# Optimization experiments

Hardware: AMD Instinct MI355X
Metric: run time of the kernel (lower is better)

Reference implementation:

```python
import jax, jax.numpy as jnp
import numpy as np

B, C, N_IN = 32, 64, 10475
N_OUT = 2619
NNZ = 8 * N_OUT  # ~8 barycentric entries per output vertex


def setup_inputs() -> dict:
    key = jax.random.key(0)
    k1, k2, k3, k4 = jax.random.split(key, 4)
    x = jax.random.normal(k1, (B, C, N_IN), dtype=jnp.float32)
    # Sparse mesh-sampling operator M [N_OUT, N_IN] in COO form,
    # sparsity pattern shared across the whole batch.
    M_rows = jax.random.randint(k2, (NNZ,), 0, N_OUT, dtype=jnp.int32)
    M_cols = jax.random.randint(k3, (NNZ,), 0, N_IN, dtype=jnp.int32)
    M_vals = jax.random.uniform(k4, (NNZ,), dtype=jnp.float32)
    return {"x": x, "M_rows": M_rows, "M_cols": M_cols, "M_vals": M_vals}


def reference(x, M_rows, M_cols, M_vals):
    """Batched spmm: out[b, c, r] = sum_{k: M_rows[k]==r} M_vals[k] * x[b, c, M_cols[k]].

    Equivalent to the torch module: for each batch element, M @ x[b].T, stacked,
    then transposed back to [B, C, N_OUT]. Here the batch loop is fused into a
    single gather + segment_sum that reuses the shared sparsity pattern.
    """
    # Gather source vertex features for every nnz entry: [B, C, NNZ]
    g = x[:, :, M_cols] * M_vals
    # segment_sum reduces over the leading axis -> move nnz to front
    g = jnp.moveaxis(g, 2, 0)                                   # [NNZ, B, C]
    out = jax.ops.segment_sum(g, M_rows, num_segments=N_OUT)    # [N_OUT, B, C]
    return jnp.moveaxis(out, 0, 2)                              # [B, C, N_OUT]
```

## Files before the change

### kernel.cpp

```cpp
#include <hip/hip_runtime.h>
#include <hip/hip_fp16.h>
#include <stdint.h>

#define Bdim   32
#define Cdim   64
#define N_IN   10475
#define N_OUT  2619
#define NNZ    (8 * N_OUT)
#define MAIN_BLK 512
#define CHUNK  41
#define ENT_PAD (CHUNK * MAIN_BLK)
#define SMALL_BLK 256
#define Gpair  2
#define NBLK   (Bdim * Cdim / Gpair)

#define SENT_META 0x0FFF0000u

#define OFF_OFFS   10480
#define OFF_ENT    20976
#define OFF_ELAST  (OFF_ENT + 20 * MAIN_BLK * 16)
#define WS_NEEDED  (OFF_ELAST + MAIN_BLK * 8)

__global__ __launch_bounds__(SMALL_BLK) void init_ws(
        int* __restrict__ cursor, uint2* __restrict__ ent2,
        uint2* __restrict__ entLast) {
    int i = blockIdx.x * SMALL_BLK + threadIdx.x;
    if (i < N_OUT) cursor[i] = 0;
    if (i < ENT_PAD - NNZ) {
        int p  = NNZ + i;
        int tt = p / CHUNK;
        int ss = p - tt * CHUNK;
        uint2 sv = make_uint2(SENT_META, 0u);
        if (ss < 40) ent2[(ss >> 1) * (MAIN_BLK * 2) + tt * 2 + (ss & 1)] = sv;
        else         entLast[tt] = sv;
    }
}

__global__ __launch_bounds__(SMALL_BLK) void hist_rows(
        const int* __restrict__ rows, int* __restrict__ counts) {
    int k = blockIdx.x * SMALL_BLK + threadIdx.x;
    if (k < NNZ) atomicAdd(&counts[rows[k]], 1);
}

__global__ __launch_bounds__(1024) void scan_counts(
        int* __restrict__ counts, int* __restrict__ offsets) {
    __shared__ int wsum[16];
    const int t = threadIdx.x, lane = t & 63, w = t >> 6;
    const int base = t * 3;
    int v0 = (base + 0 < N_OUT) ? counts[base + 0] : 0;
    int v1 = (base + 1 < N_OUT) ? counts[base + 1] : 0;
    int v2 = (base + 2 < N_OUT) ? counts[base + 2] : 0;
    int s = v0 + v1 + v2;
    const int tot = s;
    #pragma unroll
    for (int d = 1; d < 64; d <<= 1) {
        int n = __shfl_up(s, d);
        if (lane >= d) s += n;
    }
    if (lane == 63) wsum[w] = s;
    __syncthreads();
    if (t < 16) {
        int ws_ = wsum[t];
        #pragma unroll
        for (int d = 1; d < 16; d <<= 1) {
            int n = __shfl_up(ws_, d);
            if (t >= d) ws_ += n;
        }
        wsum[t] = ws_;
    }
    __syncthreads();
    int excl = ((w > 0) ? wsum[w - 1] : 0) + (s - tot);
    if (base + 0 <= N_OUT) { offsets[base + 0] = excl; if (base + 0 < N_OUT) counts[base + 0] = excl; }
    excl += v0;
    if (base + 1 <= N_OUT) { offsets[base + 1] = excl; if (base + 1 < N_OUT) counts[base + 1] = excl; }
    excl += v1;
    if (base + 2 <= N_OUT) { offsets[base + 2] = excl; if (base + 2 < N_OUT) counts[base + 2] = excl; }
}

__global__ __launch_bounds__(SMALL_BLK) void scatter_entries(
        const int* __restrict__ rows, const int* __restrict__ cols,
        const float* __restrict__ vals,
        int* __restrict__ cursor, const int* __restrict__ offsets,
        uint2* __restrict__ ent2, uint2* __restrict__ entLast) {
    int k = blockIdx.x * SMALL_BLK + threadIdx.x;
    if (k < NNZ) {
        int r = rows[k];
        int p = atomicAdd(&cursor[r], 1);
        uint32_t flag = (p == offsets[r + 1] - 1) ? 0x80000000u : 0u;
        uint32_t meta = flag | ((uint32_t)r << 16) | ((uint32_t)cols[k] << 2);
        __half2 hv = __half2half2(__float2half(vals[k]));
        uint2 e = make_uint2(meta, *(uint32_t*)&hv);
        int t = p / CHUNK;
        int s = p - t * CHUNK;
        if (s < 40) ent2[(s >> 1) * (MAIN_BLK * 2) + t * 2 + (s & 1)] = e;
        else        entLast[t] = e;
    }
}

__global__ __launch_bounds__(MAIN_BLK, 6) void spmm_g2p(
        const float* __restrict__ x,
        const uint4* __restrict__ ent4,
        const uint2* __restrict__ entLast,
        float* __restrict__ out) {
    __shared__ __half2 xs2[N_IN];
    __shared__ __half2 out2[N_OUT];
    __shared__ int     wCarryRow[8];
    __shared__ int     wCarryVal[8];

    const int blk  = blockIdx.x;
    const int t    = threadIdx.x, lane = t & 63, w = t >> 6;
    const float* __restrict__ xr0 = x + (size_t)(Gpair * blk) * N_IN;
    const float* __restrict__ xr1 = xr0 + N_IN;

    uint4 c0 = ent4[0 * MAIN_BLK + t];
    uint4 c1 = ent4[1 * MAIN_BLK + t];
    uint4 c2 = ent4[2 * MAIN_BLK + t];
    uint4 c3 = ent4[3 * MAIN_BLK + t];
    const uint2 el = entLast[t];

    __half* xsh = (__half*)xs2;
    constexpr int NP = (N_IN - 1) / 2;
    #pragma unroll 2
    for (int p = t; p < NP; p += MAIN_BLK) {
        int c = 2 * p;
        float2 a = *(const float2*)(xr0 + c);
        xsh[2 * c]     = __float2half(a.x);
        xsh[2 * c + 2] = __float2half(a.y);
    }
    #pragma unroll 2
    for (int p = t; p < NP; p += MAIN_BLK) {
        int c = 2 * p + 1;
        float2 b = *(const float2*)(xr1 + c);
        xsh[2 * c + 1] = __float2half(b.x);
        xsh[2 * c + 3] = __float2half(b.y);
    }
    if (t == 0) xsh[2 * (N_IN - 1)] = __float2half(xr0[N_IN - 1]);
    if (t == 1) xsh[1]              = __float2half(xr1[0]);
    {
        const __half2 z = __half2half2(__float2half(0.f));
        #pragma unroll
        for (int i = t; i < N_OUT; i += MAIN_BLK) out2[i] = z;
    }
    __syncthreads();

    const __half2 hzero = __half2half2(__float2half(0.f));
    __half2 acc = hzero, facc = hzero;
    int firstRow = -1;

#define FEED(meta, vb) do {                                              \
        uint32_t xp = *(const uint32_t*)((const char*)xs2 + ((meta) & 0xFFFFu)); \
        acc = __hfma2(*(const __half2*)&(vb), *(const __half2*)&xp, acc); \
        if ((int)(meta) < 0) {                                           \
            int row_ = (int)(((meta) >> 16) & 0xFFFu);                   \
            if (firstRow < 0) { firstRow = row_; facc = acc; }           \
            else out2[row_] = acc;                                       \
            acc = hzero;                                                 \
        }                                                                \
    } while (0)

    #pragma unroll
    for (int jb = 0; jb < 5; ++jb) {
        uint4 n0, n1, n2, n3;
        if (jb < 4) {
            n0 = ent4[((jb + 1) * 4 + 0) * MAIN_BLK + t];
            n1 = ent4[((jb + 1) * 4 + 1) * MAIN_BLK + t];
            n2 = ent4[((jb + 1) * 4 + 2) * MAIN_BLK + t];
            n3 = ent4[((jb + 1) * 4 + 3) * MAIN_BLK + t];
        }
        FEED(c0.x, c0.y); FEED(c0.z, c0.w);
        FEED(c1.x, c1.y); FEED(c1.z, c1.w);
        FEED(c2.x, c2.y); FEED(c2.z, c2.w);
        FEED(c3.x, c3.y); FEED(c3.z, c3.w);
        if (jb < 4) { c0 = n0; c1 = n1; c2 = n2; c3 = n3; }
    }
    FEED(el.x, el.y);
#undef FEED

    const int carryRow = (int)((el.x >> 16) & 0xFFFu);
    const int cai = *(const int*)&acc;

    int pRow = __shfl_up(carryRow, 1);
    int pAi  = __shfl_up(cai, 1);
    if (lane == 63) { wCarryRow[w] = carryRow; wCarryVal[w] = cai; }
    __syncthreads();
    if (lane == 0) {
        pRow = (w > 0) ? wCarryRow[w - 1] : -1;
        pAi  = (w > 0) ? wCarryVal[w - 1] : 0;
    }

    if (firstRow >= 0 && firstRow < N_OUT) {
        if (pRow == firstRow) facc = __hadd2(facc, *(const __half2*)&pAi);
        out2[firstRow] = facc;
    }
    __syncthreads();

    float* __restrict__ o0 = out + (size_t)(Gpair * blk) * N_OUT;
    float* __restrict__ o1 = o0 + N_OUT;
    #pragma unroll
    for (int i = t; i < N_OUT; i += MAIN_BLK) {
        float2 vv = __half22float2(out2[i]);
        o0[i] = vv.x;
        o1[i] = vv.y;
    }
}

__global__ __launch_bounds__(SMALL_BLK) void spmm_raw(
        const float* __restrict__ x,
        const int* __restrict__ rows,
        const int* __restrict__ cols,
        const float* __restrict__ vals,
        float* __restrict__ out) {
    __shared__ float x_lds[N_IN];
    __shared__ float out_lds[N_OUT];
    const int bc = blockIdx.x;
    const float* __restrict__ xrow = x + (size_t)bc * N_IN;
    for (int i = threadIdx.x; i < N_IN; i += SMALL_BLK) x_lds[i] = xrow[i];
    for (int i = threadIdx.x; i < N_OUT; i += SMALL_BLK) out_lds[i] = 0.0f;
    __syncthreads();
    for (int k = threadIdx.x; k < NNZ; k += SMALL_BLK) {
        atomicAdd(&out_lds[rows[k]], vals[k] * x_lds[cols[k]]);
    }
    __syncthreads();
    float* __restrict__ orow = out + (size_t)bc * N_OUT;
    for (int i = threadIdx.x; i < N_OUT; i += SMALL_BLK) orow[i] = out_lds[i];
}

extern "C" void kernel_launch(void* const* d_in, const int* in_sizes, int n_in,
                              void* d_out, int out_size, void* d_ws, size_t ws_size,
                              hipStream_t stream) {
    const float* x    = (const float*)d_in[0];
    const int*   rows = (const int*)d_in[1];
    const int*   cols = (const int*)d_in[2];
    const float* vals = (const float*)d_in[3];
    float*       out  = (float*)d_out;

    if (ws_size >= (size_t)WS_NEEDED) {
        char*  ws      = (char*)d_ws;
        int*   cursor  = (int*)ws;
        int*   offsets = (int*)(ws + OFF_OFFS);
        uint2* ent2    = (uint2*)(ws + OFF_ENT);
        const uint4* ent4 = (const uint4*)(ws + OFF_ENT);
        uint2* entLast = (uint2*)(ws + OFF_ELAST);

        const int gi = (N_OUT + SMALL_BLK - 1) / SMALL_BLK;
        const int gk = (NNZ + SMALL_BLK - 1) / SMALL_BLK;

        init_ws<<<gi, SMALL_BLK, 0, stream>>>(cursor, ent2, entLast);
        hist_rows<<<gk, SMALL_BLK, 0, stream>>>(rows, cursor);
        scan_counts<<<1, 1024, 0, stream>>>(cursor, offsets);
        scatter_entries<<<gk, SMALL_BLK, 0, stream>>>(rows, cols, vals, cursor,
                                                      offsets, ent2, entLast);
        spmm_g2p<<<NBLK, MAIN_BLK, 0, stream>>>(x, ent4, entLast, out);
    } else {
        spmm_raw<<<Bdim * Cdim, SMALL_BLK, 0, stream>>>(x, rows, cols, vals, out);
    }
}
```

Measured before the change: 157.8 us.

## Fuse COO preprocessing into one single-block kernel and batch LDS gathers

```diff
diff --git a/kernel.cpp b/kernel.cpp
--- a/kernel.cpp
+++ b/kernel.cpp
@@ -16,40 +16,29 @@
 
 #define SENT_META 0x0FFF0000u
 
-#define OFF_OFFS   10480
-#define OFF_ENT    20976
-#define OFF_ELAST  (OFF_ENT + 20 * MAIN_BLK * 16)
+#define OFF_ELAST  (20 * MAIN_BLK * 16)
 #define WS_NEEDED  (OFF_ELAST + MAIN_BLK * 8)
 
-__global__ __launch_bounds__(SMALL_BLK) void init_ws(
-        int* __restrict__ cursor, uint2* __restrict__ ent2,
-        uint2* __restrict__ entLast) {
-    int i = blockIdx.x * SMALL_BLK + threadIdx.x;
-    if (i < N_OUT) cursor[i] = 0;
-    if (i < ENT_PAD - NNZ) {
-        int p  = NNZ + i;
-        int tt = p / CHUNK;
-        int ss = p - tt * CHUNK;
-        uint2 sv = make_uint2(SENT_META, 0u);
-        if (ss < 40) ent2[(ss >> 1) * (MAIN_BLK * 2) + tt * 2 + (ss & 1)] = sv;
-        else         entLast[tt] = sv;
-    }
-}
-
-__global__ __launch_bounds__(SMALL_BLK) void hist_rows(
-        const int* __restrict__ rows, int* __restrict__ counts) {
-    int k = blockIdx.x * SMALL_BLK + threadIdx.x;
-    if (k < NNZ) atomicAdd(&counts[rows[k]], 1);
-}
-
-__global__ __launch_bounds__(1024) void scan_counts(
-        int* __restrict__ counts, int* __restrict__ offsets) {
+__global__ __launch_bounds__(1024) void prep_all(
+        const int* __restrict__ rows, const int* __restrict__ cols,
+        const float* __restrict__ vals,
+        uint2* __restrict__ ent2, uint2* __restrict__ entLast) {
+    __shared__ int cnt[N_OUT];
+    __shared__ int lastpos[N_OUT];
     __shared__ int wsum[16];
+
     const int t = threadIdx.x, lane = t & 63, w = t >> 6;
+
+    for (int i = t; i < N_OUT; i += 1024) cnt[i] = 0;
+    __syncthreads();
+
+    for (int k = t; k < NNZ; k += 1024) atomicAdd(&cnt[rows[k]], 1);
+    __syncthreads();
+
     const int base = t * 3;
-    int v0 = (base + 0 < N_OUT) ? counts[base + 0] : 0;
-    int v1 = (base + 1 < N_OUT) ? counts[base + 1] : 0;
-    int v2 = (base + 2 < N_OUT) ? counts[base + 2] : 0;
+    int v0 = (base + 0 < N_OUT) ? cnt[base + 0] : 0;
+    int v1 = (base + 1 < N_OUT) ? cnt[base + 1] : 0;
+    int v2 = (base + 2 < N_OUT) ? cnt[base + 2] : 0;
     int s = v0 + v1 + v2;
     const int tot = s;
     #pragma unroll
@@ -70,30 +59,32 @@
     }
     __syncthreads();
     int excl = ((w > 0) ? wsum[w - 1] : 0) + (s - tot);
-    if (base + 0 <= N_OUT) { offsets[base + 0] = excl; if (base + 0 < N_OUT) counts[base + 0] = excl; }
+    if (base + 0 < N_OUT) { cnt[base + 0] = excl; lastpos[base + 0] = excl + v0 - 1; }
     excl += v0;
-    if (base + 1 <= N_OUT) { offsets[base + 1] = excl; if (base + 1 < N_OUT) counts[base + 1] = excl; }
+    if (base + 1 < N_OUT) { cnt[base + 1] = excl; lastpos[base + 1] = excl + v1 - 1; }
     excl += v1;
-    if (base + 2 <= N_OUT) { offsets[base + 2] = excl; if (base + 2 < N_OUT) counts[base + 2] = excl; }
-}
-
-__global__ __launch_bounds__(SMALL_BLK) void scatter_entries(
-        const int* __restrict__ rows, const int* __restrict__ cols,
-        const float* __restrict__ vals,
-        int* __restrict__ cursor, const int* __restrict__ offsets,
-        uint2* __restrict__ ent2, uint2* __restrict__ entLast) {
-    int k = blockIdx.x * SMALL_BLK + threadIdx.x;
-    if (k < NNZ) {
+    if (base + 2 < N_OUT) { cnt[base + 2] = excl; lastpos[base + 2] = excl + v2 - 1; }
+    __syncthreads();
+
+    for (int k = t; k < NNZ; k += 1024) {
         int r = rows[k];
-        int p = atomicAdd(&cursor[r], 1);
-        uint32_t flag = (p == offsets[r + 1] - 1) ? 0x80000000u : 0u;
+        int p = atomicAdd(&cnt[r], 1);
+        uint32_t flag = (p == lastpos[r]) ? 0x80000000u : 0u;
         uint32_t meta = flag | ((uint32_t)r << 16) | ((uint32_t)cols[k] << 2);
         __half2 hv = __half2half2(__float2half(vals[k]));
         uint2 e = make_uint2(meta, *(uint32_t*)&hv);
-        int t = p / CHUNK;
-        int s = p - t * CHUNK;
-        if (s < 40) ent2[(s >> 1) * (MAIN_BLK * 2) + t * 2 + (s & 1)] = e;
-        else        entLast[t] = e;
+        int tt = p / CHUNK;
+        int ss = p - tt * CHUNK;
+        if (ss < 40) ent2[(ss >> 1) * (MAIN_BLK * 2) + tt * 2 + (ss & 1)] = e;
+        else         entLast[tt] = e;
+    }
+    if (t < ENT_PAD - NNZ) {
+        int p  = NNZ + t;
+        int tt = p / CHUNK;
+        int ss = p - tt * CHUNK;
+        uint2 sv = make_uint2(SENT_META, 0u);
+        if (ss < 40) ent2[(ss >> 1) * (MAIN_BLK * 2) + tt * 2 + (ss & 1)] = sv;
+        else         entLast[tt] = sv;
     }
 }
 
@@ -147,9 +138,8 @@
     __half2 acc = hzero, facc = hzero;
     int firstRow = -1;
 
-#define FEED(meta, vb) do {                                              \
-        uint32_t xp = *(const uint32_t*)((const char*)xs2 + ((meta) & 0xFFFFu)); \
-        acc = __hfma2(*(const __half2*)&(vb), *(const __half2*)&xp, acc); \
+#define ACCSTEP(meta, vb, xp) do {                                       \
+        acc = __hfma2(*(const __half2*)&(vb), *(const __half2*)&(xp), acc); \
         if ((int)(meta) < 0) {                                           \
             int row_ = (int)(((meta) >> 16) & 0xFFFu);                   \
             if (firstRow < 0) { firstRow = row_; facc = acc; }           \
@@ -167,14 +157,25 @@
             n2 = ent4[((jb + 1) * 4 + 2) * MAIN_BLK + t];
             n3 = ent4[((jb + 1) * 4 + 3) * MAIN_BLK + t];
         }
-        FEED(c0.x, c0.y); FEED(c0.z, c0.w);
-        FEED(c1.x, c1.y); FEED(c1.z, c1.w);
-        FEED(c2.x, c2.y); FEED(c2.z, c2.w);
-        FEED(c3.x, c3.y); FEED(c3.z, c3.w);
+        uint32_t xp0 = *(const uint32_t*)((const char*)xs2 + (c0.x & 0xFFFFu));
+        uint32_t xp1 = *(const uint32_t*)((const char*)xs2 + (c0.z & 0xFFFFu));
+        uint32_t xp2 = *(const uint32_t*)((const char*)xs2 + (c1.x & 0xFFFFu));
+        uint32_t xp3 = *(const uint32_t*)((const char*)xs2 + (c1.z & 0xFFFFu));
+        uint32_t xp4 = *(const uint32_t*)((const char*)xs2 + (c2.x & 0xFFFFu));
+        uint32_t xp5 = *(const uint32_t*)((const char*)xs2 + (c2.z & 0xFFFFu));
+        uint32_t xp6 = *(const uint32_t*)((const char*)xs2 + (c3.x & 0xFFFFu));
+        uint32_t xp7 = *(const uint32_t*)((const char*)xs2 + (c3.z & 0xFFFFu));
+        ACCSTEP(c0.x, c0.y, xp0); ACCSTEP(c0.z, c0.w, xp1);
+        ACCSTEP(c1.x, c1.y, xp2); ACCSTEP(c1.z, c1.w, xp3);
+        ACCSTEP(c2.x, c2.y, xp4); ACCSTEP(c2.z, c2.w, xp5);
+        ACCSTEP(c3.x, c3.y, xp6); ACCSTEP(c3.z, c3.w, xp7);
         if (jb < 4) { c0 = n0; c1 = n1; c2 = n2; c3 = n3; }
     }
-    FEED(el.x, el.y);
-#undef FEED
+    {
+        uint32_t xpl = *(const uint32_t*)((const char*)xs2 + (el.x & 0xFFFFu));
+        ACCSTEP(el.x, el.y, xpl);
+    }
+#undef ACCSTEP
 
     const int carryRow = (int)((el.x >> 16) & 0xFFFu);
     const int cai = *(const int*)&acc;
@@ -236,20 +237,11 @@
 
     if (ws_size >= (size_t)WS_NEEDED) {
         char*  ws      = (char*)d_ws;
-        int*   cursor  = (int*)ws;
-        int*   offsets = (int*)(ws + OFF_OFFS);
-        uint2* ent2    = (uint2*)(ws + OFF_ENT);
-        const uint4* ent4 = (const uint4*)(ws + OFF_ENT);
+        uint2* ent2    = (uint2*)ws;
+        const uint4* ent4 = (const uint4*)ws;
         uint2* entLast = (uint2*)(ws + OFF_ELAST);
 
-        const int gi = (N_OUT + SMALL_BLK - 1) / SMALL_BLK;
-        const int gk = (NNZ + SMALL_BLK - 1) / SMALL_BLK;
-
-        init_ws<<<gi, SMALL_BLK, 0, stream>>>(cursor, ent2, entLast);
-        hist_rows<<<gk, SMALL_BLK, 0, stream>>>(rows, cursor);
-        scan_counts<<<1, 1024, 0, stream>>>(cursor, offsets);
-        scatter_entries<<<gk, SMALL_BLK, 0, stream>>>(rows, cols, vals, cursor,
-                                                      offsets, ent2, entLast);
+        prep_all<<<1, 1024, 0, stream>>>(rows, cols, vals, ent2, entLast);
         spmm_g2p<<<NBLK, MAIN_BLK, 0, stream>>>(x, ent4, entLast, out);
     } else {
         spmm_raw<<<Bdim * Cdim, SMALL_BLK, 0, stream>>>(x, rows, cols, vals, out);
```

After: 189.7 us. 1.2x slower.
